# Performance work log

Hardware: AMD Instinct MI355X
Metric: run time of the kernel (lower is better)

Reference implementation:

```python
import jax, jax.numpy as jnp
import numpy as np

N, E, G, K, C = 16000, 256000, 64, 10, 32
NB, MH, NP, NE, ND, SH, RH = 8, 16, 4, 3, 6, 9, 64
R_MAX, AVG_NBR, P = 5.0, 16.0, 6
LVALS = jnp.array([0, 1, 1, 1, 2, 2, 2, 2, 2])  # l of each lm slot (l<=2)


def _silu(x):
    return x * jax.nn.sigmoid(x)


def _sph(v):
    # real spherical harmonics up to l=2 on unit vectors, e3nn 'component' normalization
    x, y, z = v[:, 0], v[:, 1], v[:, 2]
    s3, s5, s15 = 3.0 ** 0.5, 5.0 ** 0.5, 15.0 ** 0.5
    return jnp.stack([
        jnp.ones_like(x),
        s3 * x, s3 * y, s3 * z,
        s15 * x * y, s15 * y * z, 0.5 * s5 * (3.0 * z * z - 1.0),
        s15 * x * z, 0.5 * s15 * (x * x - y * y)], axis=-1)


def setup_inputs():
    key = jax.random.key(0)
    ks = jax.random.split(key, 26)

    def w(k, shape):
        fan_in = shape[-2] if len(shape) > 1 else shape[-1]
        return jax.random.normal(k, shape, jnp.float32) / np.float32(np.sqrt(fan_in))

    elems = jax.random.randint(ks[0], (N,), 0, K)
    return {
        'positions': 2.0 * jax.random.normal(ks[1], (N, 3), jnp.float32),
        'node_attrs': jax.nn.one_hot(elems, K, dtype=jnp.float32),
        'shifts': jnp.zeros((E, 3), jnp.float32),
        'E0': jax.random.normal(ks[2], (K,), jnp.float32),
        'W_embed': w(ks[3], (K, C)),
        'W_up': w(ks[4], (2, C, C)),
        'W_r1': w(ks[5], (2, NB, RH)),
        'W_r2': w(ks[6], (2, RH, RH)),
        'W_r3': w(ks[7], (2, RH, SH * C)),
        'W_sc': w(ks[8], (2, K, 3, C, C)),
        'W_prod': w(ks[9], (2, 3, C, C)),
        'Wc': w(ks[10], (2, 3, K, C, C)),
        'We1': w(ks[11], (2, C, MH)),
        'We2': w(ks[12], (2, MH, NE)),
        'Wi1': w(ks[13], (2, C, MH)),
        'Wi2': w(ks[14], (2, MH, NP)),
        'Wdp': w(ks[15], (2, C, ND)),
        'Wd1': w(ks[16], (NP, RH)),
        'bd1': jnp.zeros((RH,), jnp.float32),
        'Wd2': w(ks[17], (RH, NE)),
        'bd2': jnp.zeros((NE,), jnp.float32),
        'edge_index': jax.random.randint(ks[18], (2, E), 0, N).astype(jnp.int32),
        'batch': jnp.sort(jax.random.randint(ks[19], (N,), 0, G)).astype(jnp.int32),
    }


def _forward(edge_index, batch, positions, node_attrs, shifts, E0, W_embed, W_up,
             W_r1, W_r2, W_r3, W_sc, W_prod, Wc, We1, We2, Wi1, Wi2, Wdp,
             Wd1, bd1, Wd2, bd2):
    src, dst = edge_index[0], edge_index[1]
    vec = positions[src] - positions[dst] + shifts          # [E,3]
    r = jnp.sqrt(jnp.sum(vec * vec, axis=-1) + 1e-12)       # [E]
    sh = _sph(vec / r[:, None])                              # [E,9]
    # Bessel radial basis with polynomial cutoff envelope (p=6)
    u = r / R_MAX
    n = jnp.arange(1, NB + 1, dtype=jnp.float32)
    bess = jnp.sqrt(2.0 / R_MAX) * jnp.sin(n * jnp.pi * u[:, None]) / r[:, None]
    env = (1.0 - 0.5 * (P + 1) * (P + 2) * u ** P + P * (P + 2) * u ** (P + 1)
           - 0.5 * P * (P + 1) * u ** (P + 2))
    env = jnp.where(u < 1.0, env, 0.0)
    edge_feats = bess * env[:, None]                         # [E,NB]

    e0 = jax.ops.segment_sum(node_attrs @ E0, batch, num_segments=G)  # [G]
    feats = jnp.zeros((N, SH, C), jnp.float32).at[:, 0, :].set(node_attrs @ W_embed)

    eng_sum = jnp.zeros((G, NE), jnp.float32)
    inv_sum = jnp.zeros((G, NP), jnp.float32)
    dip_sum = jnp.zeros((G, 3, ND), jnp.float32)
    for l in range(2):
        up = feats[:, 0, :] @ W_up[l]                        # [N,C]
        Rw = _silu(edge_feats @ W_r1[l])
        Rw = _silu(Rw @ W_r2[l])
        Rw = (Rw @ W_r3[l]).reshape(E, SH, C)                # per-edge TP weights
        msg = Rw * sh[:, :, None] * up[src][:, None, :]      # [E,9,C]
        agg = jax.ops.segment_sum(msg, dst, num_segments=N) / AVG_NBR
        sc = jnp.einsum('nk,klcd,nlc->nld', node_attrs, W_sc[l][:, LVALS], feats)
        mixed = jnp.einsum('nlc,lcd->nld', agg, W_prod[l][LVALS])
        new = mixed + sc
        s0 = new[:, 0, :]
        # element-dependent symmetric-contraction on invariants (correlation 3)
        corr = (jnp.einsum('nk,kcd,nc->nd', node_attrs, Wc[l, 0], s0)
                + jnp.einsum('nk,kcd,nc->nd', node_attrs, Wc[l, 1], s0 * s0)
                + jnp.einsum('nk,kcd,nc->nd', node_attrs, Wc[l, 2], s0 * s0 * s0))
        feats = new.at[:, 0, :].add(corr)
        s = feats[:, 0, :]
        v = feats[:, 1:4, :]                                  # l=1 block [N,3,C]
        node_E = _silu(s @ We1[l]) @ We2[l]                   # [N,NE]
        node_inv = _silu(s @ Wi1[l]) @ Wi2[l]                 # [N,NP]
        node_dip = jnp.einsum('nvc,cd->nvd', v, Wdp[l])       # [N,3,ND]
        eng_sum = eng_sum + jax.ops.segment_sum(node_E, batch, num_segments=G)
        inv_sum = inv_sum + jax.ops.segment_sum(node_inv, batch, num_segments=G)
        dip_sum = dip_sum + jax.ops.segment_sum(node_dip, batch, num_segments=G)

    decoded = _silu(inv_sum @ Wd1 + bd1) @ Wd2 + bd2 + e0[:, None]   # [G,NE]
    total_e = eng_sum + e0[:, None]                                   # [G,NE]
    dip = jnp.transpose(dip_sum, (0, 2, 1))                           # [G,ND,3]
    return jnp.concatenate([decoded, total_e, dip.reshape(G, 3 * ND)], axis=-1)


def reference(positions, node_attrs, shifts, E0, W_embed, W_up, W_r1, W_r2, W_r3,
              W_sc, W_prod, Wc, We1, We2, Wi1, Wi2, Wdp, Wd1, bd1, Wd2, bd2,
              edge_index, batch):
    return _forward(edge_index, batch, positions, node_attrs, shifts, E0, W_embed,
                    W_up, W_r1, W_r2, W_r3, W_sc, W_prod, Wc, We1, We2, Wi1, Wi2,
                    Wdp, Wd1, bd1, Wd2, bd2)
```

## Files before the change

### kernel.cpp

```cpp
#include <hip/hip_runtime.h>
#include <math.h>

#define NN 16000
#define EE 256000
#define GG 64
#define KK 10
#define CC 32
#define NBB 8
#define MHH 16
#define NPP 4
#define NEE 3
#define NDD 6
#define SHH 9
#define RHH 64
#define SHCC (SHH*CC)

typedef __attribute__((ext_vector_type(8))) short s8b;
typedef __attribute__((ext_vector_type(4))) float f32x4;

__device__ __forceinline__ float siluf(float x){ return x / (1.0f + __expf(-x)); }
__device__ __forceinline__ short bf16rne(float x){
  unsigned u = __float_as_uint(x);
  unsigned r = u + 0x7FFFu + ((u>>16)&1u);
  return (short)(r>>16);
}

__global__ __launch_bounds__(256) void init_kernel(
    const float* __restrict__ attrs, const float* __restrict__ E0v,
    const float* __restrict__ Wemb, const int* __restrict__ batch,
    int* __restrict__ kidx, float* __restrict__ feats, float* __restrict__ e0g)
{
  int t = blockIdx.x*blockDim.x + threadIdx.x;
  if (t >= NN*CC) return;
  int n = t >> 5, d = t & 31;
  const float* a = attrs + n*KK;
  int k = 0; float best = a[0];
  #pragma unroll
  for (int j=1;j<KK;j++){ float v=a[j]; if (v>best){best=v;k=j;} }
  float* f = feats + n*SHCC;
  f[d] = Wemb[k*CC+d];
  #pragma unroll
  for (int s=1;s<SHH;s++) f[s*CC+d] = 0.0f;
  if (d==0){ kidx[n]=k; atomicAdd(&e0g[batch[n]], E0v[k]); }
}

__global__ __launch_bounds__(256) void up_kernel(
    const float* __restrict__ feats, const float* __restrict__ Wup,
    float* __restrict__ up)
{
  int t = blockIdx.x*blockDim.x + threadIdx.x;
  if (t >= NN*CC) return;
  int n = t >> 5, d = t & 31;
  const float* f = feats + n*SHCC;
  float acc = 0.0f;
  #pragma unroll
  for (int c=0;c<CC;c++) acc += f[c]*Wup[c*CC+d];
  up[t] = acc * 0.0625f;
}

__global__ __launch_bounds__(256) void hist_kernel(
    const int* __restrict__ ei, int* __restrict__ rowptr)
{
  int e = blockIdx.x*256 + threadIdx.x;
  if (e < EE) atomicAdd(&rowptr[ei[EE+e]+1], 1);
}

__global__ __launch_bounds__(1024) void scan_kernel(
    int* __restrict__ rowptr, int* __restrict__ cursor)
{
  __shared__ int part[1024];
  const int t = threadIdx.x;
  const int SEG = 16;
  const int base = t*SEG;
  int a[SEG];
  int run = 0;
  #pragma unroll
  for (int i=0;i<SEG;i++){
    int idx = base+i;
    int v = (idx <= NN) ? rowptr[idx] : 0;
    run += v; a[i] = run;
  }
  part[t] = run;
  __syncthreads();
  for (int off=1; off<1024; off<<=1){
    int v = (t>=off) ? part[t-off] : 0;
    __syncthreads();
    part[t] += v;
    __syncthreads();
  }
  int offset = (t>0) ? part[t-1] : 0;
  #pragma unroll
  for (int i=0;i<SEG;i++){
    int idx = base+i;
    if (idx <= NN){
      int val = offset + a[i];
      rowptr[idx] = val;
      if (idx < NN) cursor[idx] = val;
    }
  }
}

__global__ __launch_bounds__(256) void scatter_kernel(
    const int* __restrict__ ei, int* __restrict__ cursor, int* __restrict__ sorted)
{
  int e = blockIdx.x*256 + threadIdx.x;
  if (e < EE){
    int d = ei[EE+e];
    int p = atomicAdd(&cursor[d], 1);
    sorted[p] = e;
  }
}

__global__ __launch_bounds__(256, 2) void edge_kernel(
    const float* __restrict__ pos, const float* __restrict__ shifts,
    const float* __restrict__ Wr1, const float* __restrict__ Wr2,
    const float* __restrict__ Wr3, const float* __restrict__ up,
    const int* __restrict__ ei, const int* __restrict__ sorted,
    float* __restrict__ agg)
{
  __shared__ alignas(16) short sW3T[SHCC*RHH];
  __shared__ alignas(16) short sW2T[RHH*RHH];
  __shared__ alignas(16) float sW1T[RHH*NBB];
  __shared__ alignas(16) float ef_l[4][16*8];
  __shared__ alignas(16) float sh_l[4][16*12];
  __shared__ alignas(16) short h2s_l[4][16*72];
  __shared__ alignas(16) float msg_l[4][16*65];
  __shared__ int dst_l[4][16];

  for (int i=threadIdx.x; i<RHH*SHCC; i+=256){
    int kk = i/SHCC, o = i - kk*SHCC;
    sW3T[(o*RHH + kk) ^ ((o&7)<<3)] = bf16rne(Wr3[i]);
  }
  for (int i=threadIdx.x; i<RHH*RHH; i+=256){
    int k = i>>6, kk = i&63;
    sW2T[(kk*RHH + k) ^ ((kk&7)<<3)] = bf16rne(Wr2[i]);
  }
  for (int i=threadIdx.x; i<NBB*RHH; i+=256){
    int b = i>>6, k = i&63;
    sW1T[k*NBB + b] = Wr1[i];
  }
  __syncthreads();

  const int lane = threadIdx.x & 63;
  const int el   = lane & 15;
  const int r    = lane >> 4;
  const int wv   = threadIdx.x >> 6;
  float* efw = ef_l[wv];
  float* shw = sh_l[wv];
  short* h2w = h2s_l[wv];
  float* msg = msg_l[wv];
  int*   dstL = dst_l[wv];
  const int wid = blockIdx.x*4 + wv;
  const int nw  = gridDim.x*4;
  const f32x4 zf = {0.f,0.f,0.f,0.f};
  const float PI_ = 3.14159265358979323846f;

  for (int tile = wid; tile < EE/16; tile += nw) {
    const int e0 = tile*16;
    {
      const int e = sorted[e0 + el];
      const int src = ei[e], dst = ei[EE+e];
      if (r==0) dstL[el] = dst;
      float x = pos[src*3+0]-pos[dst*3+0]+shifts[e*3+0];
      float y = pos[src*3+1]-pos[dst*3+1]+shifts[e*3+1];
      float z = pos[src*3+2]-pos[dst*3+2]+shifts[e*3+2];
      float rr = sqrtf(x*x+y*y+z*z+1e-12f);
      float ir = 1.0f/rr;
      x*=ir; y*=ir; z*=ir;
      const float S3=1.7320508075688772f, S5h=1.1180339887498949f;
      const float S15=3.872983346207417f, S15h=1.9364916731037085f;
      if (r==0){ shw[el*12+0]=1.0f;            shw[el*12+1]=S3*x;     shw[el*12+2]=S3*y; }
      else if (r==1){ shw[el*12+3]=S3*z;       shw[el*12+4]=S15*x*y;  shw[el*12+5]=S15*y*z; }
      else if (r==2){ shw[el*12+6]=S5h*(3.0f*z*z-1.0f); shw[el*12+7]=S15*x*z; shw[el*12+8]=S15h*(x*x-y*y); }
      float u = rr*0.2f;
      float u2=u*u, u3=u2*u, u6=u3*u3;
      float env = 1.0f - 28.0f*u6 + 48.0f*u6*u - 21.0f*u6*u2;
      env = (u<1.0f)? env : 0.0f;
      env *= ir * 0.6324555320336759f;
      float n1 = (float)(r+1), n2 = (float)(r+5);
      efw[el*8 + r]     = __sinf(n1*PI_*u)*env;
      efw[el*8 + r + 4] = __sinf(n2*PI_*u)*env;
    }
    float h1v[16];
    {
      f32x4 efa = *(const f32x4*)&efw[el*8];
      f32x4 efb = *(const f32x4*)&efw[el*8+4];
      #pragma unroll
      for (int s=0;s<2;s++){
        #pragma unroll
        for (int j=0;j<8;j++){
          int kq = 32*s + 8*r + j;
          f32x4 wa = *(const f32x4*)&sW1T[kq*NBB];
          f32x4 wb = *(const f32x4*)&sW1T[kq*NBB+4];
          float acc = efa[0]*wa[0]+efa[1]*wa[1]+efa[2]*wa[2]+efa[3]*wa[3]
                    + efb[0]*wb[0]+efb[1]*wb[1]+efb[2]*wb[2]+efb[3]*wb[3];
          h1v[s*8+j] = siluf(acc);
        }
      }
    }
    s8b a1s0, a1s1;
    #pragma unroll
    for (int j=0;j<8;j++){ a1s0[j]=bf16rne(h1v[j]); a1s1[j]=bf16rne(h1v[8+j]); }

    f32x4 aw2[4];
    #pragma unroll
    for (int t=0;t<4;t++){
      int kk = 16*t + el;
      int sw = (kk&7)<<3;
      s8b b0 = *(const s8b*)&sW2T[(kk*RHH + 8*r     ) ^ sw];
      s8b b1 = *(const s8b*)&sW2T[(kk*RHH + 8*r + 32) ^ sw];
      f32x4 acc = __builtin_amdgcn_mfma_f32_16x16x32_bf16(a1s0, b0, zf, 0,0,0);
      aw2[t]    = __builtin_amdgcn_mfma_f32_16x16x32_bf16(a1s1, b1, acc, 0,0,0);
    }
    #pragma unroll
    for (int t=0;t<4;t++){
      #pragma unroll
      for (int reg=0;reg<4;reg++)
        h2w[(4*r+reg)*72 + 16*t + el] = bf16rne(siluf(aw2[t][reg]));
    }
    s8b a2s0 = *(const s8b*)&h2w[el*72 + 8*r];
    s8b a2s1 = *(const s8b*)&h2w[el*72 + 32 + 8*r];

    float upv[4][2];
    #pragma unroll
    for (int reg=0;reg<4;reg++){
      int ee = sorted[e0 + 4*r + reg];
      int s_ = ei[ee];
      upv[reg][0] = up[s_*CC + el];
      upv[reg][1] = up[s_*CC + 16 + el];
    }
    #pragma unroll
    for (int c=0;c<5;c++){
      const int tBeg = 4*c;
      const int tEnd = (c<4)? (4*c+4) : 18;
      #pragma unroll
      for (int t=tBeg;t<tEnd;t++){
        int o = 16*t + el;
        int sw = (o&7)<<3;
        s8b b0 = *(const s8b*)&sW3T[(o*RHH + 8*r     ) ^ sw];
        s8b b1 = *(const s8b*)&sW3T[(o*RHH + 8*r + 32) ^ sw];
        f32x4 acc = __builtin_amdgcn_mfma_f32_16x16x32_bf16(a2s0, b0, zf, 0,0,0);
        acc       = __builtin_amdgcn_mfma_f32_16x16x32_bf16(a2s1, b1, acc, 0,0,0);
        const int sidx = t>>1, spar = t&1;
        #pragma unroll
        for (int reg=0;reg<4;reg++){
          int e = 4*r + reg;
          float v = acc[reg] * shw[e*12 + sidx] * upv[reg][spar];
          msg[e*65 + 16*(t-tBeg) + el] = v;
        }
      }
      const int colIdx = (c<4) ? lane : (lane & 31);
      const bool active = (c<4) || (lane < 32);
      const int obase = 64*c;
      int i = 0;
      while (i < 16){
        int d = dstL[i];
        float a = msg[i*65 + colIdx];
        int j = i+1;
        while (j < 16 && dstL[j]==d){ a += msg[j*65 + colIdx]; j++; }
        if (active) atomicAdd(agg + (size_t)d*SHCC + obase + colIdx, a);
        i = j;
      }
    }
  }
}

__global__ __launch_bounds__(256) void node_kernel(
    const float* __restrict__ feats, float* __restrict__ fout,
    const float* __restrict__ agg,
    const int* __restrict__ kidx, const int* __restrict__ batch,
    const float* __restrict__ Wsc, const float* __restrict__ Wprod,
    const float* __restrict__ WcL,
    const float* __restrict__ We1, const float* __restrict__ We2,
    const float* __restrict__ Wi1, const float* __restrict__ Wi2,
    const float* __restrict__ Wdp,
    float* __restrict__ eng, float* __restrict__ inv, float* __restrict__ dip)
{
  __shared__ float s0l[8][CC];
  __shared__ float sul[8][CC];
  __shared__ float vl[8][3][CC];
  __shared__ float hl[8][CC];
  const int t = threadIdx.x;
  const int nn = t >> 5;
  const int d = t & 31;
  const int n = blockIdx.x*8 + nn;
  const int k = kidx[n];
  const int b = batch[n];
  const float* fin = feats + n*SHCC;
  const float* ag = agg + n*SHCC;
  float nw[SHH];
  const int LV[SHH] = {0,1,1,1,2,2,2,2,2};
  #pragma unroll
  for (int s=0;s<SHH;s++){
    const int lv = LV[s];
    const float* wp  = Wprod + lv*CC*CC + d;
    const float* wsc = Wsc + (k*3+lv)*CC*CC + d;
    float acc = 0.0f;
    #pragma unroll
    for (int c=0;c<CC;c++)
      acc += ag[s*CC+c]*wp[c*CC] + fin[s*CC+c]*wsc[c*CC];
    nw[s] = acc;
  }
  s0l[nn][d] = nw[0];
  vl[nn][0][d] = nw[1]; vl[nn][1][d] = nw[2]; vl[nn][2][d] = nw[3];
  __syncthreads();
  float corr = 0.0f;
  {
    const float* wc0 = WcL + (0*KK+k)*CC*CC + d;
    const float* wc1 = WcL + (1*KK+k)*CC*CC + d;
    const float* wc2 = WcL + (2*KK+k)*CC*CC + d;
    #pragma unroll
    for (int c=0;c<CC;c++){
      float s0 = s0l[nn][c];
      float s2 = s0*s0;
      corr += s0*wc0[c*CC] + s2*wc1[c*CC] + s2*s0*wc2[c*CC];
    }
  }
  float su = nw[0] + corr;
  sul[nn][d] = su;
  float* fo = fout + n*SHCC;
  fo[d] = su;
  #pragma unroll
  for (int s=1;s<SHH;s++) fo[s*CC+d] = nw[s];
  __syncthreads();
  {
    const int m = d & 15;
    const float* W = (d < MHH) ? We1 : Wi1;
    float acc = 0.0f;
    #pragma unroll
    for (int c=0;c<CC;c++) acc += sul[nn][c]*W[c*MHH+m];
    hl[nn][d] = siluf(acc);
  }
  __syncthreads();
  if (d < NEE){
    float acc=0.0f;
    #pragma unroll
    for (int m=0;m<MHH;m++) acc += hl[nn][m]*We2[m*NEE+d];
    atomicAdd(&eng[b*NEE+d], acc);
  } else if (d < NEE+NPP){
    const int p = d-NEE;
    float acc=0.0f;
    #pragma unroll
    for (int m=0;m<MHH;m++) acc += hl[nn][MHH+m]*Wi2[m*NPP+p];
    atomicAdd(&inv[b*NPP+p], acc);
  } else if (d < 7+3*NDD){
    const int idx = d-7;
    const int v = idx/NDD;
    const int dd = idx - v*NDD;
    float acc=0.0f;
    #pragma unroll
    for (int c=0;c<CC;c++) acc += vl[nn][v][c]*Wdp[c*NDD+dd];
    atomicAdd(&dip[(b*3+v)*NDD+dd], acc);
  }
}

__global__ __launch_bounds__(64) void final_kernel(
    const float* __restrict__ eng, const float* __restrict__ inv,
    const float* __restrict__ dip, const float* __restrict__ e0g,
    const float* __restrict__ Wd1, const float* __restrict__ bd1,
    const float* __restrict__ Wd2, const float* __restrict__ bd2,
    float* __restrict__ out)
{
  const int g = threadIdx.x;
  if (g >= GG) return;
  float e0 = e0g[g];
  float iv0=inv[g*NPP+0], iv1=inv[g*NPP+1], iv2=inv[g*NPP+2], iv3=inv[g*NPP+3];
  float o0=bd2[0], o1=bd2[1], o2=bd2[2];
  for (int m=0;m<RHH;m++){
    float hm = bd1[m] + iv0*Wd1[0*RHH+m] + iv1*Wd1[1*RHH+m] + iv2*Wd1[2*RHH+m] + iv3*Wd1[3*RHH+m];
    hm = siluf(hm);
    o0 += hm*Wd2[m*NEE+0]; o1 += hm*Wd2[m*NEE+1]; o2 += hm*Wd2[m*NEE+2];
  }
  float* og = out + g*24;
  og[0]=o0+e0; og[1]=o1+e0; og[2]=o2+e0;
  og[3]=eng[g*NEE+0]+e0; og[4]=eng[g*NEE+1]+e0; og[5]=eng[g*NEE+2]+e0;
  for (int dd=0;dd<NDD;dd++)
    for (int v=0;v<3;v++)
      og[6+dd*3+v] = dip[(g*3+v)*NDD+dd];
}

extern "C" void kernel_launch(void* const* d_in, const int* in_sizes, int n_in,
                              void* d_out, int out_size, void* d_ws, size_t ws_size,
                              hipStream_t stream)
{
  const float* pos    = (const float*)d_in[0];
  const float* attrs  = (const float*)d_in[1];
  const float* shifts = (const float*)d_in[2];
  const float* E0v    = (const float*)d_in[3];
  const float* Wemb   = (const float*)d_in[4];
  const float* Wup    = (const float*)d_in[5];
  const float* Wr1    = (const float*)d_in[6];
  const float* Wr2    = (const float*)d_in[7];
  const float* Wr3    = (const float*)d_in[8];
  const float* Wsc    = (const float*)d_in[9];
  const float* Wprod  = (const float*)d_in[10];
  const float* Wc     = (const float*)d_in[11];
  const float* We1    = (const float*)d_in[12];
  const float* We2    = (const float*)d_in[13];
  const float* Wi1    = (const float*)d_in[14];
  const float* Wi2    = (const float*)d_in[15];
  const float* Wdp    = (const float*)d_in[16];
  const float* Wd1    = (const float*)d_in[17];
  const float* bd1    = (const float*)d_in[18];
  const float* Wd2    = (const float*)d_in[19];
  const float* bd2    = (const float*)d_in[20];
  const int*   ei     = (const int*)d_in[21];
  const int*   batch  = (const int*)d_in[22];
  float* out = (float*)d_out;

  float* feats = (float*)d_ws;
  float* agg   = feats + (size_t)NN*SHCC;
  float* up    = agg   + (size_t)NN*SHCC;
  float* accum = up    + (size_t)NN*CC;
  float* e0g = accum;
  float* eng = accum + 64;
  float* inv = accum + 256;
  float* dip = accum + 512;
  int*   kidx   = (int*)(accum + 1664);
  int*   rowptr = kidx + NN;
  int*   cursor = rowptr + NN + 1;
  int*   sorted = cursor + NN;

  hipMemsetAsync(accum, 0, 1664*sizeof(float), stream);
  hipMemsetAsync(rowptr, 0, (NN+1)*sizeof(int), stream);
  init_kernel<<<(NN*CC)/256, 256, 0, stream>>>(attrs, E0v, Wemb, batch, kidx, feats, e0g);
  hist_kernel<<<EE/256, 256, 0, stream>>>(ei, rowptr);
  scan_kernel<<<1, 1024, 0, stream>>>(rowptr, cursor);
  scatter_kernel<<<EE/256, 256, 0, stream>>>(ei, cursor, sorted);

  for (int l=0; l<2; ++l){
    up_kernel<<<(NN*CC)/256, 256, 0, stream>>>(feats, Wup + l*CC*CC, up);
    hipMemsetAsync(agg, 0, (size_t)NN*SHCC*sizeof(float), stream);
    edge_kernel<<<512, 256, 0, stream>>>(pos, shifts,
        Wr1 + l*NBB*RHH, Wr2 + l*RHH*RHH, Wr3 + l*RHH*SHCC,
        up, ei, sorted, agg);
    node_kernel<<<NN/8, 256, 0, stream>>>(feats, feats, agg, kidx, batch,
        Wsc + l*KK*3*CC*CC, Wprod + l*3*CC*CC, Wc + l*3*KK*CC*CC,
        We1 + l*CC*MHH, We2 + l*MHH*NEE, Wi1 + l*CC*MHH, Wi2 + l*MHH*NPP,
        Wdp + l*CC*NDD,
        eng, inv, dip);
  }
  final_kernel<<<1, 64, 0, stream>>>(eng, inv, dip, e0g, Wd1, bd1, Wd2, bd2, out);
}
```

Measured before the change: 783.7 us.

## Fuse up-projection into init/node kernels and block-wide edge segment reduction

Removes the separate up_kernel by computing the layer-0 up projection in init_kernel and the layer-1 projection in node_kernel from the new scalar features. The edge kernel now handles 64 consecutive sorted edges per block with a shared message buffer. A ballot-derived run mask marks destination runs, and those runs are reduced and atomically added, shared across all four waves. This cuts atomics and kernel launches but adds block-wide __syncthreads per chunk. One risk: node_kernel in layer 1 also writes up with Wup1, which is unused but harmless, while layer 0 overwrites up that edge_kernel already consumed.

```diff
diff --git a/kernel.cpp b/kernel.cpp
--- a/kernel.cpp
+++ b/kernel.cpp
@@ -27,8 +27,10 @@
 
 __global__ __launch_bounds__(256) void init_kernel(
     const float* __restrict__ attrs, const float* __restrict__ E0v,
-    const float* __restrict__ Wemb, const int* __restrict__ batch,
-    int* __restrict__ kidx, float* __restrict__ feats, float* __restrict__ e0g)
+    const float* __restrict__ Wemb, const float* __restrict__ Wup0,
+    const int* __restrict__ batch,
+    int* __restrict__ kidx, float* __restrict__ feats, float* __restrict__ e0g,
+    float* __restrict__ up)
 {
   int t = blockIdx.x*blockDim.x + threadIdx.x;
   if (t >= NN*CC) return;
@@ -41,21 +43,11 @@
   f[d] = Wemb[k*CC+d];
   #pragma unroll
   for (int s=1;s<SHH;s++) f[s*CC+d] = 0.0f;
+  float accu = 0.0f;
+  #pragma unroll
+  for (int c=0;c<CC;c++) accu += Wemb[k*CC+c]*Wup0[c*CC+d];
+  up[n*CC+d] = accu * 0.0625f;
   if (d==0){ kidx[n]=k; atomicAdd(&e0g[batch[n]], E0v[k]); }
-}
-
-__global__ __launch_bounds__(256) void up_kernel(
-    const float* __restrict__ feats, const float* __restrict__ Wup,
-    float* __restrict__ up)
-{
-  int t = blockIdx.x*blockDim.x + threadIdx.x;
-  if (t >= NN*CC) return;
-  int n = t >> 5, d = t & 31;
-  const float* f = feats + n*SHCC;
-  float acc = 0.0f;
-  #pragma unroll
-  for (int c=0;c<CC;c++) acc += f[c]*Wup[c*CC+d];
-  up[t] = acc * 0.0625f;
 }
 
 __global__ __launch_bounds__(256) void hist_kernel(
@@ -121,11 +113,9 @@
   __shared__ alignas(16) short sW3T[SHCC*RHH];
   __shared__ alignas(16) short sW2T[RHH*RHH];
   __shared__ alignas(16) float sW1T[RHH*NBB];
-  __shared__ alignas(16) float ef_l[4][16*8];
+  __shared__ alignas(16) char  uni[64*65*4];
   __shared__ alignas(16) float sh_l[4][16*12];
-  __shared__ alignas(16) short h2s_l[4][16*72];
-  __shared__ alignas(16) float msg_l[4][16*65];
-  __shared__ int dst_l[4][16];
+  __shared__ int dst_l[64];
 
   for (int i=threadIdx.x; i<RHH*SHCC; i+=256){
     int kk = i/SHCC, o = i - kk*SHCC;
@@ -141,26 +131,24 @@
   }
   __syncthreads();
 
-  const int lane = threadIdx.x & 63;
+  const int tid  = threadIdx.x;
+  const int lane = tid & 63;
   const int el   = lane & 15;
   const int r    = lane >> 4;
-  const int wv   = threadIdx.x >> 6;
-  float* efw = ef_l[wv];
+  const int wv   = tid >> 6;
+  float* msg = (float*)uni;
+  float* efw = (float*)(uni + wv*512);
+  short* h2w = (short*)(uni + 2048 + wv*2304);
   float* shw = sh_l[wv];
-  short* h2w = h2s_l[wv];
-  float* msg = msg_l[wv];
-  int*   dstL = dst_l[wv];
-  const int wid = blockIdx.x*4 + wv;
-  const int nw  = gridDim.x*4;
   const f32x4 zf = {0.f,0.f,0.f,0.f};
   const float PI_ = 3.14159265358979323846f;
 
-  for (int tile = wid; tile < EE/16; tile += nw) {
-    const int e0 = tile*16;
+  for (int w = blockIdx.x; w < EE/64; w += gridDim.x) {
+    const int e0 = w*64 + wv*16;
     {
       const int e = sorted[e0 + el];
       const int src = ei[e], dst = ei[EE+e];
-      if (r==0) dstL[el] = dst;
+      if (r==0) dst_l[wv*16+el] = dst;
       float x = pos[src*3+0]-pos[dst*3+0]+shifts[e*3+0];
       float y = pos[src*3+1]-pos[dst*3+1]+shifts[e*3+1];
       float z = pos[src*3+2]-pos[dst*3+2]+shifts[e*3+2];
@@ -229,11 +217,18 @@
       upv[reg][0] = up[s_*CC + el];
       upv[reg][1] = up[s_*CC + 16 + el];
     }
+    __syncthreads();
+
+    unsigned long long runmask;
+    {
+      bool flag = (lane==0) || (dst_l[lane] != dst_l[lane-1]);
+      runmask = __ballot(flag);
+    }
+
     #pragma unroll
     for (int c=0;c<5;c++){
       const int tBeg = 4*c;
-      const int tEnd = (c<4)? (4*c+4) : 18;
-      #pragma unroll
+      const int tEnd = (c<4)? (tBeg+4) : 18;
       for (int t=tBeg;t<tEnd;t++){
         int o = 16*t + el;
         int sw = (o&7)<<3;
@@ -244,23 +239,33 @@
         const int sidx = t>>1, spar = t&1;
         #pragma unroll
         for (int reg=0;reg<4;reg++){
-          int e = 4*r + reg;
-          float v = acc[reg] * shw[e*12 + sidx] * upv[reg][spar];
-          msg[e*65 + 16*(t-tBeg) + el] = v;
+          float v = acc[reg] * shw[(4*r+reg)*12 + sidx] * upv[reg][spar];
+          msg[(wv*16 + 4*r + reg)*65 + 16*(t-tBeg) + el] = v;
         }
       }
-      const int colIdx = (c<4) ? lane : (lane & 31);
-      const bool active = (c<4) || (lane < 32);
-      const int obase = 64*c;
-      int i = 0;
-      while (i < 16){
-        int d = dstL[i];
-        float a = msg[i*65 + colIdx];
-        int j = i+1;
-        while (j < 16 && dstL[j]==d){ a += msg[j*65 + colIdx]; j++; }
-        if (active) atomicAdd(agg + (size_t)d*SHCC + obase + colIdx, a);
-        i = j;
+      __syncthreads();
+      {
+        const int col = (c<4) ? (tid & 63) : (tid & 31);
+        const bool act = (c<4) || ((tid & 63) < 32);
+        const int q = tid >> 6;
+        const int obase = 64*c;
+        if (act){
+          unsigned long long m = runmask;
+          int j = 0;
+          while (m){
+            int s = __builtin_ctzll(m);
+            m &= (m-1);
+            int en = m ? __builtin_ctzll(m) : 64;
+            if ((j & 3) == q){
+              float a = 0.0f;
+              for (int i=s;i<en;i++) a += msg[i*65 + col];
+              atomicAdd(agg + (size_t)dst_l[s]*SHCC + obase + col, a);
+            }
+            j++;
+          }
+        }
       }
+      __syncthreads();
     }
   }
 }
@@ -273,7 +278,8 @@
     const float* __restrict__ WcL,
     const float* __restrict__ We1, const float* __restrict__ We2,
     const float* __restrict__ Wi1, const float* __restrict__ Wi2,
-    const float* __restrict__ Wdp,
+    const float* __restrict__ Wdp, const float* __restrict__ Wup1,
+    float* __restrict__ up,
     float* __restrict__ eng, float* __restrict__ inv, float* __restrict__ dip)
 {
   __shared__ float s0l[8][CC];
@@ -330,6 +336,12 @@
     #pragma unroll
     for (int c=0;c<CC;c++) acc += sul[nn][c]*W[c*MHH+m];
     hl[nn][d] = siluf(acc);
+  }
+  {
+    float acc = 0.0f;
+    #pragma unroll
+    for (int c=0;c<CC;c++) acc += sul[nn][c]*Wup1[c*CC+d];
+    up[n*CC+d] = acc * 0.0625f;
   }
   __syncthreads();
   if (d < NEE){
@@ -423,13 +435,12 @@
 
   hipMemsetAsync(accum, 0, 1664*sizeof(float), stream);
   hipMemsetAsync(rowptr, 0, (NN+1)*sizeof(int), stream);
-  init_kernel<<<(NN*CC)/256, 256, 0, stream>>>(attrs, E0v, Wemb, batch, kidx, feats, e0g);
+  init_kernel<<<(NN*CC)/256, 256, 0, stream>>>(attrs, E0v, Wemb, Wup, batch, kidx, feats, e0g, up);
   hist_kernel<<<EE/256, 256, 0, stream>>>(ei, rowptr);
   scan_kernel<<<1, 1024, 0, stream>>>(rowptr, cursor);
   scatter_kernel<<<EE/256, 256, 0, stream>>>(ei, cursor, sorted);
 
   for (int l=0; l<2; ++l){
-    up_kernel<<<(NN*CC)/256, 256, 0, stream>>>(feats, Wup + l*CC*CC, up);
     hipMemsetAsync(agg, 0, (size_t)NN*SHCC*sizeof(float), stream);
     edge_kernel<<<512, 256, 0, stream>>>(pos, shifts,
         Wr1 + l*NBB*RHH, Wr2 + l*RHH*RHH, Wr3 + l*RHH*SHCC,
@@ -437,7 +448,7 @@
     node_kernel<<<NN/8, 256, 0, stream>>>(feats, feats, agg, kidx, batch,
         Wsc + l*KK*3*CC*CC, Wprod + l*3*CC*CC, Wc + l*3*KK*CC*CC,
         We1 + l*CC*MHH, We2 + l*MHH*NEE, Wi1 + l*CC*MHH, Wi2 + l*MHH*NPP,
-        Wdp + l*CC*NDD,
+        Wdp + l*CC*NDD, Wup + 1*CC*CC, up,
         eng, inv, dip);
   }
   final_kernel<<<1, 64, 0, stream>>>(eng, inv, dip, e0g, Wd1, bd1, Wd2, bd2, out);
```

New measurement: 767.3 us. 2.1% less time.
